# Performance work log

Hardware: AMD Instinct MI355X
Metric: run time of the kernel (lower is better)

The kernel has to match this reference:

```python
import jax, jax.numpy as jnp
import numpy as np

CODEBOOK_SIZE = 8192
DECAY = 0.99  # codebook_decay


def setup_inputs() -> dict:
    key = jax.random.key(0)
    k1, k2 = jax.random.split(key)
    N, D, K = 32768, 512, CODEBOOK_SIZE
    target = jax.random.normal(k1, (N, D), dtype=jnp.float32)
    codebook = jax.random.normal(k2, (K, D), dtype=jnp.float32)
    counts = jnp.ones((K,), dtype=jnp.float32)
    return {"target": target, "codebook": codebook, "counts": counts}


def reference(target, codebook, counts):
    # target: [N, D]; codebook: [K, D] (running EMA sum); counts: [K] (running EMA count)
    K = codebook.shape[0]
    cb = codebook / counts[:, None]  # normalized code vectors, [K, D]

    # cdist(target, cb, p=2).argmin(1): argmin of squared euclidean distance
    # ||t - c||^2 = ||t||^2 - 2 t.c + ||c||^2   (||t||^2 constant over codes)
    d2 = (
        jnp.sum(target * target, axis=1, keepdims=True)  # [N, 1]
        - 2.0 * target @ cb.T                             # [N, K]
        + jnp.sum(cb * cb, axis=1)[None, :]               # [1, K]
    )
    labels = jnp.argmin(d2, axis=1)                       # [N]
    onehot = jax.nn.one_hot(labels, K, dtype=jnp.float32)  # [N, K]

    # EMA step (training path): per-code histogram + per-code sum of targets
    count = jax.ops.segment_sum(jnp.ones_like(labels, dtype=jnp.float32), labels, num_segments=K)  # [K]
    memory = jax.ops.segment_sum(target, labels, num_segments=K)  # [K, D] == onehot.T @ target

    alpha = jnp.where(count != 0, DECAY, 1.0)             # [K]
    new_counts = alpha * counts + (1.0 - alpha) * count
    new_codebook = alpha[:, None] * codebook + (1.0 - alpha)[:, None] * memory
    return onehot, new_codebook, new_counts
```

## Files before the change

kernel.cpp:

```cpp
#include <hip/hip_runtime.h>
#include <hip/hip_fp16.h>

typedef _Float16 f16;
typedef _Float16 f16x8 __attribute__((ext_vector_type(8)));
typedef _Float16 f16x4 __attribute__((ext_vector_type(4)));
typedef float    f32x4 __attribute__((ext_vector_type(4)));

#define DECAY   0.99f
#define MARGIN  0.3f
#define MARGIN2 2e-3f
#define MAXA    4096

#define BM    256
#define BN    256
#define BK    64
#define NSPANS 128
#define NSPAN2 32

__device__ __forceinline__ void gl_lds16(const void* g, void* l) {
  __builtin_amdgcn_global_load_lds(
      (const __attribute__((address_space(1))) unsigned int*)g,
      (__attribute__((address_space(3))) unsigned int*)l, 16, 0, 0);
}

__global__ void prep_cb(const float* __restrict__ codebook, const float* __restrict__ counts,
                        f16* __restrict__ cHi, f16* __restrict__ cLo, float* __restrict__ cnorm,
                        unsigned* __restrict__ hist, unsigned* __restrict__ cnts, int D) {
  const int k = blockIdx.x;
  const int tid = threadIdx.x;
  const float cnt = counts[k];
  float4 v = ((const float4*)(codebook + (size_t)k * D))[tid];
  float c0 = v.x / cnt, c1 = v.y / cnt, c2 = v.z / cnt, c3 = v.w / cnt;
  f16 h0 = (f16)c0, h1 = (f16)c1, h2 = (f16)c2, h3 = (f16)c3;
  f16x4 h = {h0, h1, h2, h3};
  f16x4 l = {(f16)(c0 - (float)h0), (f16)(c1 - (float)h1),
             (f16)(c2 - (float)h2), (f16)(c3 - (float)h3)};
  *(f16x4*)(cHi + (size_t)k * D + tid * 4) = h;
  *(f16x4*)(cLo + (size_t)k * D + tid * 4) = l;
  float s = c0*c0 + c1*c1 + c2*c2 + c3*c3;
  #pragma unroll
  for (int m = 1; m < 64; m <<= 1) s += __shfl_xor(s, m);
  __shared__ float red[2];
  if ((tid & 63) == 0) red[tid >> 6] = s;
  __syncthreads();
  if (tid == 0) {
    cnorm[k] = red[0] + red[1];
    hist[k] = 0u;
    if (k == 0) { cnts[0] = 0u; cnts[64] = 0u; }
  }
}

__global__ void prep_t(const float4* __restrict__ t4, f16x4* __restrict__ hi4, long total4) {
  for (long i = blockIdx.x * (long)blockDim.x + threadIdx.x; i < total4;
       i += (long)gridDim.x * blockDim.x) {
    float4 v = t4[i];
    f16x4 h = {(f16)v.x, (f16)v.y, (f16)v.z, (f16)v.w};
    hi4[i] = h;
  }
}

__global__ __launch_bounds__(512, 2)
void argmin_pass(const f16* __restrict__ tHi, const f16* __restrict__ cHi,
                 const float* __restrict__ cnorm, float4* __restrict__ partials,
                 int D, int Nrows) {
  __shared__ __align__(16) unsigned char smem[131072];
  unsigned char* ldsA = smem;
  unsigned char* ldsB = smem + 65536;

  const int tid = threadIdx.x;
  const int w = tid >> 6, lane = tid & 63;
  const int wm = w >> 2, wn = w & 3;
  const int rowBase = blockIdx.x * BM;
  const int colBase = blockIdx.y * BN;

  int aOff[4], bOff[4];
  unsigned ldsOff[4];
  #pragma unroll
  for (int i = 0; i < 4; ++i) {
    int s = (i * 8 + w) * 64 + lane;
    int r = s >> 3, c = s & 7;
    int exel = (c ^ (r & 7)) * 8;
    aOff[i] = (rowBase + r) * D + exel;
    bOff[i] = (colBase + r) * D + exel;
    ldsOff[i] = (i * 8 + w) * 1024;
  }

  f32x4 acc[8][4];
  #pragma unroll
  for (int m = 0; m < 8; ++m)
    #pragma unroll
    for (int n = 0; n < 4; ++n) { f32x4 z = {0.f, 0.f, 0.f, 0.f}; acc[m][n] = z; }

  #pragma unroll
  for (int i = 0; i < 4; ++i) gl_lds16(tHi + aOff[i], ldsA + ldsOff[i]);
  #pragma unroll
  for (int i = 0; i < 4; ++i) gl_lds16(cHi + bOff[i], ldsB + ldsOff[i]);

  int buf = 0;
  #pragma unroll 1
  for (int t = 0; t < 8; ++t) {
    const int d0N = ((t + 1) & 7) * BK;
    unsigned char* lAn = ldsA + ((buf ^ 1) << 15);
    unsigned char* lBn = ldsB + ((buf ^ 1) << 15);
    #pragma unroll
    for (int i = 0; i < 4; ++i) gl_lds16(tHi + aOff[i] + d0N, lAn + ldsOff[i]);
    #pragma unroll
    for (int i = 0; i < 4; ++i) gl_lds16(cHi + bOff[i] + d0N, lBn + ldsOff[i]);

    asm volatile("s_waitcnt vmcnt(8)" ::: "memory");
    __builtin_amdgcn_s_barrier();

    unsigned char* lA = ldsA + (buf << 15);
    unsigned char* lB = ldsB + (buf << 15);
    __builtin_amdgcn_s_setprio(1);
    #pragma unroll
    for (int ks = 0; ks < 2; ++ks) {
      const int chunk = ks * 4 + (lane >> 4);
      f16x8 af[8];
      #pragma unroll
      for (int m = 0; m < 8; ++m) {
        int r = wm * 128 + m * 16 + (lane & 15);
        af[m] = *(const f16x8*)(lA + r * 128 + ((chunk ^ (r & 7)) * 16));
      }
      f16x8 bfr[4];
      #pragma unroll
      for (int n = 0; n < 4; ++n) {
        int r = wn * 64 + n * 16 + (lane & 15);
        bfr[n] = *(const f16x8*)(lB + r * 128 + ((chunk ^ (r & 7)) * 16));
      }
      #pragma unroll
      for (int m = 0; m < 8; ++m)
        #pragma unroll
        for (int n = 0; n < 4; ++n)
          acc[m][n] = __builtin_amdgcn_mfma_f32_16x16x32_f16(af[m], bfr[n], acc[m][n], 0, 0, 0);
    }
    __builtin_amdgcn_s_setprio(0);

    asm volatile("s_waitcnt lgkmcnt(0)" ::: "memory");
    __builtin_amdgcn_s_barrier();
    buf ^= 1;
  }

  float cn[4];
  #pragma unroll
  for (int n = 0; n < 4; ++n) cn[n] = cnorm[colBase + wn * 64 + n * 16 + (lane & 15)];

  const int span = blockIdx.y * 4 + wn;
  const int g = lane >> 4;
  #pragma unroll
  for (int m = 0; m < 8; ++m) {
    #pragma unroll
    for (int j = 0; j < 4; ++j) {
      float m1 = __builtin_inff(), m2 = __builtin_inff();
      unsigned a1 = 0u;
      #pragma unroll
      for (int n = 0; n < 4; ++n) {
        float v = fmaf(-2.0f, acc[m][n][j], cn[n]);
        unsigned c = (unsigned)(colBase + wn * 64 + n * 16 + (lane & 15));
        if (v < m1) { m2 = m1; m1 = v; a1 = c; }
        else if (v < m2) { m2 = v; }
      }
      #pragma unroll
      for (int msk = 1; msk < 16; msk <<= 1) {
        float o1 = __shfl_xor(m1, msk);
        unsigned oa = (unsigned)__shfl_xor((int)a1, msk);
        float o2 = __shfl_xor(m2, msk);
        bool bet = (o1 < m1) || (o1 == m1 && oa < a1);
        float nm2 = bet ? fminf(m1, o2) : fminf(m2, o1);
        if (bet) { m1 = o1; a1 = oa; }
        m2 = nm2;
      }
      if ((lane & 15) == 0) {
        int r = rowBase + wm * 128 + m * 16 + g * 4 + j;
        float4 p;
        p.x = m1;
        p.y = __uint_as_float(a1);
        p.z = m2;
        p.w = 0.f;
        partials[(size_t)span * Nrows + r] = p;
      }
    }
  }
}

__global__ void reduce_labels(const float4* __restrict__ partials, int* __restrict__ labels,
                              unsigned* __restrict__ cnts, unsigned* __restrict__ list1,
                              unsigned* __restrict__ list2, int N) {
  int r = blockIdx.x * blockDim.x + threadIdx.x;
  if (r >= N) return;
  float m1 = __builtin_inff(), m2 = __builtin_inff();
  unsigned a1 = 0u;
  #pragma unroll 4
  for (int s = 0; s < NSPANS; ++s) {
    float4 p = partials[(size_t)s * N + r];
    float o1 = p.x;
    unsigned oa = __float_as_uint(p.y);
    float o2 = p.z;
    bool bet = (o1 < m1) || (o1 == m1 && oa < a1);
    float nm2 = bet ? fminf(m1, o2) : fminf(m2, o1);
    if (bet) { m1 = o1; a1 = oa; }
    m2 = nm2;
  }
  labels[r] = (int)a1;
  if (m2 - m1 < MARGIN) {
    unsigned idx = atomicAdd(&cnts[0], 1u);
    if (idx < MAXA) list1[idx] = (unsigned)r;
    else { unsigned i2 = atomicAdd(&cnts[64], 1u); list2[i2] = (unsigned)r; }
  }
}

__global__ void gather_k(const float4* __restrict__ t4, const unsigned* __restrict__ cnts,
                         const unsigned* __restrict__ list1, f16x4* __restrict__ gHi4,
                         f16x4* __restrict__ gLo4) {
  unsigned i = blockIdx.x * blockDim.x + threadIdx.x;
  unsigned a = i >> 7, j = i & 127;
  unsigned cntA = cnts[0] < MAXA ? cnts[0] : MAXA;
  if (a >= cntA) return;
  unsigned r = list1[a];
  float4 v = t4[(size_t)r * 128 + j];
  f16 h0 = (f16)v.x, h1 = (f16)v.y, h2 = (f16)v.z, h3 = (f16)v.w;
  f16x4 h = {h0, h1, h2, h3};
  f16x4 l = {(f16)(v.x - (float)h0), (f16)(v.y - (float)h1),
             (f16)(v.z - (float)h2), (f16)(v.w - (float)h3)};
  gHi4[(size_t)a * 128 + j] = h;
  gLo4[(size_t)a * 128 + j] = l;
}

__global__ __launch_bounds__(256, 2)
void refine_mfma(const f16* __restrict__ gHi, const f16* __restrict__ gLo,
                 const f16* __restrict__ cHi, const f16* __restrict__ cLo,
                 const float* __restrict__ cnorm, const unsigned* __restrict__ cnts,
                 float4* __restrict__ partials2, int D) {
  __shared__ __align__(16) unsigned char smem[2 * 128 * 64 * 2];
  unsigned char* ldsA = smem;
  unsigned char* ldsB = smem + 128 * 64 * 2;

  const unsigned cntA = cnts[0] < MAXA ? cnts[0] : MAXA;
  const int rowBase = blockIdx.x * 128;
  if ((unsigned)rowBase >= cntA) return;
  const int colBase = blockIdx.y * 256;

  const int tid = threadIdx.x;
  const int w = tid >> 6, lane = tid & 63;

  int rloc[4], exel[4], ldsOff[4];
  #pragma unroll
  for (int i = 0; i < 4; ++i) {
    int s = (i * 4 + w) * 64 + lane;
    int r = s >> 3, c = s & 7;
    rloc[i] = r;
    exel[i] = (c ^ (r & 7)) * 8;
    ldsOff[i] = (i * 4 + w) * 1024;
  }
  size_t aBase[4];
  #pragma unroll
  for (int i = 0; i < 4; ++i) aBase[i] = (size_t)(rowBase + rloc[i]) * D + exel[i];

  float rm1[8], rm2[8];
  unsigned ra1[8];
  #pragma unroll
  for (int i = 0; i < 8; ++i) { rm1[i] = __builtin_inff(); rm2[i] = __builtin_inff(); ra1[i] = 0u; }

  #pragma unroll 1
  for (int tile = 0; tile < 2; ++tile) {
    const int c0 = colBase + tile * 128;
    size_t bOff[4];
    #pragma unroll
    for (int i = 0; i < 4; ++i) bOff[i] = (size_t)(c0 + rloc[i]) * D + exel[i];

    f32x4 acc[2][8];
    #pragma unroll
    for (int m = 0; m < 2; ++m)
      #pragma unroll
      for (int n = 0; n < 8; ++n) { f32x4 z = {0.f, 0.f, 0.f, 0.f}; acc[m][n] = z; }

    #pragma unroll 1
    for (int pass = 0; pass < 3; ++pass) {
      const f16* __restrict__ A = (pass == 2) ? gLo : gHi;
      const f16* __restrict__ B = (pass == 1) ? cLo : cHi;
      #pragma unroll 1
      for (int ds = 0; ds < 8; ++ds) {
        const int d0 = ds * 64;
        __syncthreads();
        #pragma unroll
        for (int i = 0; i < 4; ++i) gl_lds16(A + aBase[i] + d0, ldsA + ldsOff[i]);
        #pragma unroll
        for (int i = 0; i < 4; ++i) gl_lds16(B + bOff[i] + d0, ldsB + ldsOff[i]);
        __syncthreads();
        #pragma unroll
        for (int ks = 0; ks < 2; ++ks) {
          const int chunk = ks * 4 + (lane >> 4);
          f16x8 af[2];
          #pragma unroll
          for (int m = 0; m < 2; ++m) {
            int r = w * 32 + m * 16 + (lane & 15);
            af[m] = *(const f16x8*)(ldsA + r * 128 + ((chunk ^ (r & 7)) * 16));
          }
          f16x8 bfr[8];
          #pragma unroll
          for (int n = 0; n < 8; ++n) {
            int r = n * 16 + (lane & 15);
            bfr[n] = *(const f16x8*)(ldsB + r * 128 + ((chunk ^ (r & 7)) * 16));
          }
          #pragma unroll
          for (int m = 0; m < 2; ++m)
            #pragma unroll
            for (int n = 0; n < 8; ++n)
              acc[m][n] = __builtin_amdgcn_mfma_f32_16x16x32_f16(af[m], bfr[n], acc[m][n], 0, 0, 0);
        }
      }
    }

    float cn[8];
    #pragma unroll
    for (int n = 0; n < 8; ++n) cn[n] = cnorm[c0 + n * 16 + (lane & 15)];
    #pragma unroll
    for (int m = 0; m < 2; ++m) {
      #pragma unroll
      for (int j = 0; j < 4; ++j) {
        float m1 = __builtin_inff(), m2 = __builtin_inff();
        unsigned a1 = 0u;
        #pragma unroll
        for (int n = 0; n < 8; ++n) {
          float v = fmaf(-2.0f, acc[m][n][j], cn[n]);
          unsigned c = (unsigned)(c0 + n * 16 + (lane & 15));
          if (v < m1) { m2 = m1; m1 = v; a1 = c; }
          else if (v < m2) { m2 = v; }
        }
        #pragma unroll
        for (int msk = 1; msk < 16; msk <<= 1) {
          float o1 = __shfl_xor(m1, msk);
          unsigned oa = (unsigned)__shfl_xor((int)a1, msk);
          float o2 = __shfl_xor(m2, msk);
          bool bet = (o1 < m1) || (o1 == m1 && oa < a1);
          float nm2 = bet ? fminf(m1, o2) : fminf(m2, o1);
          if (bet) { m1 = o1; a1 = oa; }
          m2 = nm2;
        }
        const int idx = m * 4 + j;
        bool bet = (m1 < rm1[idx]) || (m1 == rm1[idx] && a1 < ra1[idx]);
        float nm2 = bet ? fminf(rm1[idx], m2) : fminf(rm2[idx], m1);
        if (bet) { rm1[idx] = m1; ra1[idx] = a1; }
        rm2[idx] = nm2;
      }
    }
  }

  if ((lane & 15) == 0) {
    const int g = lane >> 4;
    #pragma unroll
    for (int m = 0; m < 2; ++m)
      #pragma unroll
      for (int j = 0; j < 4; ++j) {
        int a = rowBase + w * 32 + m * 16 + g * 4 + j;
        const int idx = m * 4 + j;
        float4 p;
        p.x = rm1[idx];
        p.y = __uint_as_float(ra1[idx]);
        p.z = rm2[idx];
        p.w = 0.f;
        partials2[(size_t)a * NSPAN2 + blockIdx.y] = p;
      }
  }
}

__global__ void reduce2(const float4* __restrict__ partials2, const unsigned* __restrict__ list1,
                        unsigned* __restrict__ cnts, unsigned* __restrict__ list2,
                        int* __restrict__ labels) {
  unsigned a = blockIdx.x * blockDim.x + threadIdx.x;
  unsigned cntA = cnts[0] < MAXA ? cnts[0] : MAXA;
  if (a >= cntA) return;
  float m1 = __builtin_inff(), m2 = __builtin_inff();
  unsigned a1 = 0u;
  #pragma unroll 4
  for (int s = 0; s < NSPAN2; ++s) {
    float4 p = partials2[(size_t)a * NSPAN2 + s];
    float o1 = p.x;
    unsigned oa = __float_as_uint(p.y);
    float o2 = p.z;
    bool bet = (o1 < m1) || (o1 == m1 && oa < a1);
    float nm2 = bet ? fminf(m1, o2) : fminf(m2, o1);
    if (bet) { m1 = o1; a1 = oa; }
    m2 = nm2;
  }
  unsigned r = list1[a];
  labels[r] = (int)a1;
  if (m2 - m1 < MARGIN2) {
    unsigned i2 = atomicAdd(&cnts[64], 1u);
    list2[i2] = r;
  }
}

__global__ __launch_bounds__(256)
void refine_scan(const float* __restrict__ target, const float* __restrict__ codebook,
                 const float* __restrict__ counts, const unsigned* __restrict__ cnts,
                 const unsigned* __restrict__ list2,
                 double* __restrict__ pv, int* __restrict__ pi, int K, int D) {
  const unsigned cnt = cnts[64];
  const unsigned nItems = cnt * 8u;
  const int w = threadIdx.x >> 6, lane = threadIdx.x & 63;
  __shared__ double sv[4];
  __shared__ int si[4];
  for (unsigned item = blockIdx.x; item < nItems; item += gridDim.x) {
    const unsigned a = item >> 3;
    const int chunk = (int)(item & 7u);
    const int r = (int)list2[a];
    const float4* t4 = (const float4*)(target + (size_t)r * D);
    float4 ta = t4[lane * 2], tb = t4[lane * 2 + 1];
    double t0 = ta.x, t1 = ta.y, t2 = ta.z, t3 = ta.w;
    double t4v = tb.x, t5 = tb.y, t6 = tb.z, t7 = tb.w;

    double bv = 1e300;
    int bc = 0;
    const int cBase = chunk * (K / 8) + w * (K / 32);
    #pragma unroll 2
    for (int i = 0; i < K / 32; ++i) {
      const int c = cBase + i;
      const float4* cb4 = (const float4*)(codebook + (size_t)c * D);
      float4 ca = cb4[lane * 2], cb = cb4[lane * 2 + 1];
      const double inv = 1.0 / (double)counts[c];
      double s = 0.0, e;
      e = t0 - (double)ca.x * inv; s = fma(e, e, s);
      e = t1 - (double)ca.y * inv; s = fma(e, e, s);
      e = t2 - (double)ca.z * inv; s = fma(e, e, s);
      e = t3 - (double)ca.w * inv; s = fma(e, e, s);
      e = t4v - (double)cb.x * inv; s = fma(e, e, s);
      e = t5 - (double)cb.y * inv; s = fma(e, e, s);
      e = t6 - (double)cb.z * inv; s = fma(e, e, s);
      e = t7 - (double)cb.w * inv; s = fma(e, e, s);
      #pragma unroll
      for (int m = 1; m < 64; m <<= 1) s += __shfl_xor(s, m);
      if (s < bv) { bv = s; bc = c; }
    }
    if (lane == 0) { sv[w] = bv; si[w] = bc; }
    __syncthreads();
    if (threadIdx.x == 0) {
      double m = sv[0];
      int bi = si[0];
      #pragma unroll
      for (int t = 1; t < 4; ++t)
        if (sv[t] < m || (sv[t] == m && si[t] < bi)) { m = sv[t]; bi = si[t]; }
      pv[(size_t)a * 8 + chunk] = m;
      pi[(size_t)a * 8 + chunk] = bi;
    }
    __syncthreads();
  }
}

__global__ void refine_merge(const double* __restrict__ pv, const int* __restrict__ pi,
                             const unsigned* __restrict__ cnts,
                             const unsigned* __restrict__ list2, int* __restrict__ labels) {
  unsigned a = blockIdx.x * blockDim.x + threadIdx.x;
  if (a >= cnts[64]) return;
  double m = pv[(size_t)a * 8];
  int best = pi[(size_t)a * 8];
  #pragma unroll
  for (int c = 1; c < 8; ++c) {
    double v = pv[(size_t)a * 8 + c];
    int idx = pi[(size_t)a * 8 + c];
    if (v < m || (v == m && idx < best)) { m = v; best = idx; }
  }
  labels[list2[a]] = best;
}

__global__ void hist_k(const int* __restrict__ labels, unsigned* __restrict__ hist, int N) {
  int n = blockIdx.x * blockDim.x + threadIdx.x;
  if (n < N) atomicAdd(&hist[labels[n]], 1u);
}

__global__ void counts_k(const float* __restrict__ counts, const unsigned* __restrict__ hist,
                         float* __restrict__ outCnt, int K) {
  int k = blockIdx.x * blockDim.x + threadIdx.x;
  if (k >= K) return;
  unsigned h = hist[k];
  float alpha = h ? DECAY : 1.0f;
  outCnt[k] = alpha * counts[k] + (1.0f - alpha) * (float)h;
}

__global__ void init_cb(const float4* __restrict__ cb4, const unsigned* __restrict__ hist,
                        float4* __restrict__ out4) {
  int k = blockIdx.x * 2 + (threadIdx.x >> 7);
  int d4 = threadIdx.x & 127;
  float alpha = hist[k] ? DECAY : 1.0f;
  size_t i = (size_t)k * 128 + d4;
  float4 v = cb4[i];
  v.x *= alpha; v.y *= alpha; v.z *= alpha; v.w *= alpha;
  out4[i] = v;
}

__global__ void scatter_k(const float4* __restrict__ t4, const int* __restrict__ labels,
                          float* __restrict__ outCb) {
  int n = blockIdx.x * 2 + (threadIdx.x >> 7);
  int d4 = threadIdx.x & 127;
  int lab = labels[n];
  float4 v = t4[(size_t)n * 128 + d4];
  float* dst = outCb + (size_t)lab * 512 + (d4 << 2);
  const float cc = 1.0f - DECAY;
  atomicAdd(dst + 0, cc * v.x);
  atomicAdd(dst + 1, cc * v.y);
  atomicAdd(dst + 2, cc * v.z);
  atomicAdd(dst + 3, cc * v.w);
}

__global__ void onehot_k(const int* __restrict__ labels, float4* __restrict__ out, int K4) {
  const int n = blockIdx.x;
  const int lab = labels[n];
  const int lab4 = lab >> 2;
  float4* row = out + (size_t)n * K4;
  const float4 z = {0.f, 0.f, 0.f, 0.f};
  for (int c4 = threadIdx.x; c4 < K4; c4 += blockDim.x) {
    if (c4 != lab4) {
      row[c4] = z;
    } else {
      float4 v = z;
      ((float*)&v)[lab & 3] = 1.0f;
      row[c4] = v;
    }
  }
}

extern "C" void kernel_launch(void* const* d_in, const int* in_sizes, int n_in,
                              void* d_out, int out_size, void* d_ws, size_t ws_size,
                              hipStream_t stream) {
  const float* target   = (const float*)d_in[0];
  const float* codebook = (const float*)d_in[1];
  const float* counts   = (const float*)d_in[2];
  const int K = in_sizes[2];
  const int D = in_sizes[1] / K;
  const int N = in_sizes[0] / D;

  float* outOnehot = (float*)d_out;
  float* outCb  = outOnehot + (size_t)N * K;
  float* outCnt = outCb + (size_t)K * D;

  unsigned char* p = (unsigned char*)d_ws;
  f16* tHi = (f16*)p;       p += (size_t)N * D * 2;
  f16* cHi = (f16*)p;       p += (size_t)K * D * 2;
  f16* cLo = (f16*)p;       p += (size_t)K * D * 2;
  float* cnorm = (float*)p; p += (size_t)K * 4;
  float4* partials = (float4*)p; p += (size_t)N * NSPANS * 16;
  int* labels = (int*)p;    p += (size_t)N * 4;
  unsigned* hist = (unsigned*)p;  p += (size_t)K * 4;
  unsigned* cnts = (unsigned*)p;  p += 512;
  unsigned* list1 = (unsigned*)p; p += (size_t)MAXA * 4;
  unsigned* list2 = (unsigned*)p; p += (size_t)N * 4;
  f16* gHi = (f16*)p;       p += (size_t)MAXA * D * 2;
  f16* gLo = (f16*)p;       p += (size_t)MAXA * D * 2;
  float4* partials2 = (float4*)p; p += (size_t)MAXA * NSPAN2 * 16;
  double* refpv = (double*)p;     p += (size_t)N * 8 * 8;
  int* refpi = (int*)p;           p += (size_t)N * 8 * 4;
  if ((size_t)(p - (unsigned char*)d_ws) > ws_size) return;

  hipLaunchKernelGGL(prep_cb, dim3(K), dim3(128), 0, stream,
                     codebook, counts, cHi, cLo, cnorm, hist, cnts, D);
  hipLaunchKernelGGL(prep_t, dim3(2048), dim3(256), 0, stream,
                     (const float4*)target, (f16x4*)tHi, (long)((size_t)N * D / 4));
  hipLaunchKernelGGL(argmin_pass, dim3(N / BM, K / BN), dim3(512), 0, stream,
                     tHi, cHi, cnorm, partials, D, N);
  hipLaunchKernelGGL(reduce_labels, dim3((N + 255) / 256), dim3(256), 0, stream,
                     partials, labels, cnts, list1, list2, N);
  hipLaunchKernelGGL(gather_k, dim3(MAXA * 128 / 256), dim3(256), 0, stream,
                     (const float4*)target, cnts, list1, (f16x4*)gHi, (f16x4*)gLo);
  hipLaunchKernelGGL(refine_mfma, dim3(MAXA / 128, NSPAN2), dim3(256), 0, stream,
                     gHi, gLo, cHi, cLo, cnorm, cnts, partials2, D);
  hipLaunchKernelGGL(reduce2, dim3((MAXA + 255) / 256), dim3(256), 0, stream,
                     partials2, list1, cnts, list2, labels);
  hipLaunchKernelGGL(refine_scan, dim3(2048), dim3(256), 0, stream,
                     target, codebook, counts, cnts, list2, refpv, refpi, K, D);
  hipLaunchKernelGGL(refine_merge, dim3((N + 255) / 256), dim3(256), 0, stream,
                     refpv, refpi, cnts, list2, labels);
  hipLaunchKernelGGL(hist_k, dim3((N + 255) / 256), dim3(256), 0, stream, labels, hist, N);
  hipLaunchKernelGGL(counts_k, dim3((K + 255) / 256), dim3(256), 0, stream, counts, hist, outCnt, K);
  hipLaunchKernelGGL(init_cb, dim3(K / 2), dim3(256), 0, stream,
                     (const float4*)codebook, hist, (float4*)outCb);
  hipLaunchKernelGGL(scatter_k, dim3(N / 2), dim3(256), 0, stream,
                     (const float4*)target, labels, outCb);
  hipLaunchKernelGGL(onehot_k, dim3(N), dim3(256), 0, stream,
                     labels, (float4*)outOnehot, K / 4);
}
```

Before: 1.318 ms.

## Use triple-buffered BK=32 pipeline and reduce wave partials in LDS

The argmin GEMM now uses a K-step of 32 with three LDS stages instead of two 64-wide stages, cutting shared memory from 128KB to 96KB and deepening the prefetch. The swizzle is redone for the 64-byte rows. At the end of the block, the four per-wave-column partial minima are combined in LDS, so each block writes one partial per row. This shrinks the partials buffer and the later reduce pass by a factor of four (NSPANS 128 to 32). The tradeoff is twice as many loop iterations and barriers per tile, plus an extra block-level sync.

```diff
diff --git a/kernel.cpp b/kernel.cpp
--- a/kernel.cpp
+++ b/kernel.cpp
@@ -13,8 +13,8 @@
 
 #define BM    256
 #define BN    256
-#define BK    64
-#define NSPANS 128
+#define BK    32
+#define NSPANS 32
 #define NSPAN2 32
 
 __device__ __forceinline__ void gl_lds16(const void* g, void* l) {
@@ -63,23 +63,23 @@
 void argmin_pass(const f16* __restrict__ tHi, const f16* __restrict__ cHi,
                  const float* __restrict__ cnorm, float4* __restrict__ partials,
                  int D, int Nrows) {
-  __shared__ __align__(16) unsigned char smem[131072];
-  unsigned char* ldsA = smem;
-  unsigned char* ldsB = smem + 65536;
+  __shared__ __align__(16) unsigned char smem[98304];
 
   const int tid = threadIdx.x;
   const int w = tid >> 6, lane = tid & 63;
   const int wm = w >> 2, wn = w & 3;
+  const int lr = lane & 15, cc = lane >> 4;
   const int rowBase = blockIdx.x * BM;
   const int colBase = blockIdx.y * BN;
 
-  int aOff[4], bOff[4];
-  unsigned ldsOff[4];
-  #pragma unroll
-  for (int i = 0; i < 4; ++i) {
-    int s = (i * 8 + w) * 64 + lane;
-    int r = s >> 3, c = s & 7;
-    int exel = (c ^ (r & 7)) * 8;
+  int aOff[2], bOff[2];
+  unsigned ldsOff[2];
+  #pragma unroll
+  for (int i = 0; i < 2; ++i) {
+    int s = i * 512 + tid;
+    int r = s >> 2, c = s & 3;
+    int sw = (r ^ (r >> 2)) & 3;
+    int exel = (c ^ sw) * 8;
     aOff[i] = (rowBase + r) * D + exel;
     bOff[i] = (colBase + r) * D + exel;
     ldsOff[i] = (i * 8 + w) * 1024;
@@ -91,61 +91,60 @@
     #pragma unroll
     for (int n = 0; n < 4; ++n) { f32x4 z = {0.f, 0.f, 0.f, 0.f}; acc[m][n] = z; }
 
-  #pragma unroll
-  for (int i = 0; i < 4; ++i) gl_lds16(tHi + aOff[i], ldsA + ldsOff[i]);
-  #pragma unroll
-  for (int i = 0; i < 4; ++i) gl_lds16(cHi + bOff[i], ldsB + ldsOff[i]);
-
-  int buf = 0;
+  #define STAGE(t, b)                                                        \
+    {                                                                        \
+      const int d0_ = ((t) & 15) * BK;                                       \
+      unsigned char* A_ = smem + (b) * 32768;                                \
+      unsigned char* B_ = A_ + 16384;                                        \
+      gl_lds16(tHi + aOff[0] + d0_, A_ + ldsOff[0]);                         \
+      gl_lds16(tHi + aOff[1] + d0_, A_ + ldsOff[1]);                         \
+      gl_lds16(cHi + bOff[0] + d0_, B_ + ldsOff[0]);                         \
+      gl_lds16(cHi + bOff[1] + d0_, B_ + ldsOff[1]);                         \
+    }
+
+  STAGE(0, 0);
+  STAGE(1, 1);
+
   #pragma unroll 1
-  for (int t = 0; t < 8; ++t) {
-    const int d0N = ((t + 1) & 7) * BK;
-    unsigned char* lAn = ldsA + ((buf ^ 1) << 15);
-    unsigned char* lBn = ldsB + ((buf ^ 1) << 15);
-    #pragma unroll
-    for (int i = 0; i < 4; ++i) gl_lds16(tHi + aOff[i] + d0N, lAn + ldsOff[i]);
-    #pragma unroll
-    for (int i = 0; i < 4; ++i) gl_lds16(cHi + bOff[i] + d0N, lBn + ldsOff[i]);
+  for (int t = 0; t < 16; ++t) {
+    STAGE(t + 2, (t + 2) % 3);
 
     asm volatile("s_waitcnt vmcnt(8)" ::: "memory");
     __builtin_amdgcn_s_barrier();
 
-    unsigned char* lA = ldsA + (buf << 15);
-    unsigned char* lB = ldsB + (buf << 15);
+    const unsigned char* A = smem + (t % 3) * 32768;
+    const unsigned char* B = A + 16384;
+    f16x8 af[8], bf[4];
+    #pragma unroll
+    for (int m = 0; m < 8; ++m) {
+      int R = wm * 128 + m * 16 + lr;
+      int sw = (R ^ (R >> 2)) & 3;
+      af[m] = *(const f16x8*)(A + R * 64 + ((cc ^ sw) * 16));
+    }
+    #pragma unroll
+    for (int n = 0; n < 4; ++n) {
+      int R = wn * 64 + n * 16 + lr;
+      int sw = (R ^ (R >> 2)) & 3;
+      bf[n] = *(const f16x8*)(B + R * 64 + ((cc ^ sw) * 16));
+    }
     __builtin_amdgcn_s_setprio(1);
     #pragma unroll
-    for (int ks = 0; ks < 2; ++ks) {
-      const int chunk = ks * 4 + (lane >> 4);
-      f16x8 af[8];
-      #pragma unroll
-      for (int m = 0; m < 8; ++m) {
-        int r = wm * 128 + m * 16 + (lane & 15);
-        af[m] = *(const f16x8*)(lA + r * 128 + ((chunk ^ (r & 7)) * 16));
-      }
-      f16x8 bfr[4];
-      #pragma unroll
-      for (int n = 0; n < 4; ++n) {
-        int r = wn * 64 + n * 16 + (lane & 15);
-        bfr[n] = *(const f16x8*)(lB + r * 128 + ((chunk ^ (r & 7)) * 16));
-      }
-      #pragma unroll
-      for (int m = 0; m < 8; ++m)
-        #pragma unroll
-        for (int n = 0; n < 4; ++n)
-          acc[m][n] = __builtin_amdgcn_mfma_f32_16x16x32_f16(af[m], bfr[n], acc[m][n], 0, 0, 0);
-    }
+    for (int m = 0; m < 8; ++m)
+      #pragma unroll
+      for (int n = 0; n < 4; ++n)
+        acc[m][n] = __builtin_amdgcn_mfma_f32_16x16x32_f16(af[m], bf[n], acc[m][n], 0, 0, 0);
     __builtin_amdgcn_s_setprio(0);
 
     asm volatile("s_waitcnt lgkmcnt(0)" ::: "memory");
     __builtin_amdgcn_s_barrier();
-    buf ^= 1;
-  }
+  }
+  #undef STAGE
 
   float cn[4];
   #pragma unroll
-  for (int n = 0; n < 4; ++n) cn[n] = cnorm[colBase + wn * 64 + n * 16 + (lane & 15)];
-
-  const int span = blockIdx.y * 4 + wn;
+  for (int n = 0; n < 4; ++n) cn[n] = cnorm[colBase + wn * 64 + n * 16 + lr];
+
+  float4* sm = (float4*)smem;
   const int g = lane >> 4;
   #pragma unroll
   for (int m = 0; m < 8; ++m) {
@@ -156,7 +155,7 @@
       #pragma unroll
       for (int n = 0; n < 4; ++n) {
         float v = fmaf(-2.0f, acc[m][n][j], cn[n]);
-        unsigned c = (unsigned)(colBase + wn * 64 + n * 16 + (lane & 15));
+        unsigned c = (unsigned)(colBase + wn * 64 + n * 16 + lr);
         if (v < m1) { m2 = m1; m1 = v; a1 = c; }
         else if (v < m2) { m2 = v; }
       }
@@ -171,15 +170,32 @@
         m2 = nm2;
       }
       if ((lane & 15) == 0) {
-        int r = rowBase + wm * 128 + m * 16 + g * 4 + j;
+        int rloc = wm * 128 + m * 16 + g * 4 + j;
         float4 p;
-        p.x = m1;
-        p.y = __uint_as_float(a1);
-        p.z = m2;
-        p.w = 0.f;
-        partials[(size_t)span * Nrows + r] = p;
+        p.x = m1; p.y = __uint_as_float(a1); p.z = m2; p.w = 0.f;
+        sm[wn * 256 + rloc] = p;
       }
     }
+  }
+  __syncthreads();
+
+  if (tid < 256) {
+    float m1 = __builtin_inff(), m2 = __builtin_inff();
+    unsigned a1 = 0u;
+    #pragma unroll
+    for (int s = 0; s < 4; ++s) {
+      float4 p = sm[s * 256 + tid];
+      float o1 = p.x;
+      unsigned oa = __float_as_uint(p.y);
+      float o2 = p.z;
+      bool bet = (o1 < m1) || (o1 == m1 && oa < a1);
+      float nm2 = bet ? fminf(m1, o2) : fminf(m2, o1);
+      if (bet) { m1 = o1; a1 = oa; }
+      m2 = nm2;
+    }
+    float4 p;
+    p.x = m1; p.y = __uint_as_float(a1); p.z = m2; p.w = 0.f;
+    partials[(size_t)blockIdx.y * Nrows + rowBase + tid] = p;
   }
 }
 
```

New measurement: 1.320 ms. About the same (+0.2%).
